# Optimization experiments

Hardware: AMD Instinct MI355X
Metric: run time of the kernel (lower is better)

Reference implementation:

```python
import jax, jax.numpy as jnp
import numpy as np

N_NODES = 100_000
N_EDGES = 2_500_000
HID = 32
SE3_NORM = 1.0 / np.sqrt(32.0)  # e3nn path normalization for 32x0e -> 32x0e


def setup_inputs() -> dict:
    key = jax.random.key(0)
    ks = jax.random.split(key, 14)
    inp = {
        "pos": jax.random.normal(ks[0], (N_NODES, 3), dtype=jnp.float32),
        "edge_index": jax.random.randint(ks[1], (2, N_EDGES), 0, N_NODES, dtype=jnp.int64),
        "Wl1": jax.random.normal(ks[2], (2, HID), dtype=jnp.float32) * 0.5,
        "bl1": jax.random.normal(ks[3], (HID,), dtype=jnp.float32) * 0.1,
        "Wr1": jax.random.normal(ks[4], (2, HID), dtype=jnp.float32) * 0.5,
        "Wl2": jax.random.normal(ks[5], (HID, HID), dtype=jnp.float32) * 0.15,
        "bl2": jax.random.normal(ks[6], (HID,), dtype=jnp.float32) * 0.1,
        "Wr2": jax.random.normal(ks[7], (HID, HID), dtype=jnp.float32) * 0.15,
        "Wse1": jax.random.normal(ks[8], (HID, HID), dtype=jnp.float32) * 0.15,
        "Wse2": jax.random.normal(ks[9], (HID, HID), dtype=jnp.float32) * 0.15,
        "W3": jax.random.normal(ks[10], (HID, HID), dtype=jnp.float32) * 0.15,
        "b3": jax.random.normal(ks[11], (HID,), dtype=jnp.float32) * 0.1,
        "W4": jax.random.normal(ks[12], (HID, 1), dtype=jnp.float32) * 0.15,
        "b4": jax.random.normal(ks[13], (1,), dtype=jnp.float32) * 0.1,
        "alpha": jnp.float32(0.5),
    }
    return inp


def _sage_conv(x, src, dst, Wl, bl, Wr, n_nodes):
    # gather messages from source nodes, scatter-sum onto destination nodes
    agg = jax.ops.segment_sum(x[src], dst, num_segments=n_nodes)  # [N, d_in]
    return agg @ Wl + bl + x @ Wr  # lin_l(agg) + lin_r(x); lin_r has no bias


def reference(pos, edge_index, Wl1, bl1, Wr1, Wl2, bl2, Wr2, Wse1, Wse2, W3, b3, W4, b4, alpha):
    n = pos.shape[0]
    x = pos[:, :2]                       # [N, 2]
    src, dst = edge_index[0], edge_index[1]

    h1 = _sage_conv(x, src, dst, Wl1, bl1, Wr1, n)   # [N, 32]
    h1 = jax.nn.leaky_relu(h1, negative_slope=0.01)  # dropout = identity (eval)
    h1 = (h1 @ Wse1) * SE3_NORM                      # SE3Linear 32x0e->32x0e

    h2 = _sage_conv(h1, src, dst, Wl2, bl2, Wr2, n)
    h2 = jax.nn.leaky_relu(h2, negative_slope=0.01)
    h2 = (h2 @ Wse2) * SE3_NORM

    x_skip = alpha * h1 + h2
    x_out = jax.nn.relu(x_skip @ W3 + b3)            # mlp3 (dropout identity)
    pred = x_out @ W4 + b4                           # mlp4
    return pred.squeeze(-1)                          # [N]
```

## Files before the change

kernel.cpp:

```cpp
#include <hip/hip_runtime.h>
#include <hip/hip_fp16.h>

#define HID 32
#define LEAKY 0.01f
#define SE3NORM 0.17677669529663687f
#define SCAN_TILE 1024
#define NBK 128
#define GA 256
#define NPB2 64


__global__ void k_bhist(const int* __restrict__ ei, int* __restrict__ bh,
                        int E, int B1, int chunk) {
    extern __shared__ int lh[];
    int g = blockIdx.x;
    for (int i = threadIdx.x; i < B1; i += 256) lh[i] = 0;
    __syncthreads();
    int beg = g * chunk, end = min(E, beg + chunk);
    for (int e = beg + (int)threadIdx.x; e < end; e += 256)
        atomicAdd(&lh[ei[E + e] >> 7], 1);
    __syncthreads();
    for (int b = threadIdx.x; b < B1; b += 256) bh[b * GA + g] = lh[b];
}

__global__ void k_scan1(int* __restrict__ data, int* __restrict__ bsum, int M) {
    __shared__ int lds[256];
    int t = threadIdx.x;
    int base = blockIdx.x * SCAN_TILE + t * 4;
    int v0 = (base + 0 < M) ? data[base + 0] : 0;
    int v1 = (base + 1 < M) ? data[base + 1] : 0;
    int v2 = (base + 2 < M) ? data[base + 2] : 0;
    int v3 = (base + 3 < M) ? data[base + 3] : 0;
    int s = v0 + v1 + v2 + v3;
    lds[t] = s;
    __syncthreads();
    for (int off = 1; off < 256; off <<= 1) {
        int x = (t >= off) ? lds[t - off] : 0;
        __syncthreads();
        lds[t] += x;
        __syncthreads();
    }
    int ex = lds[t] - s;
    if (base + 0 < M) data[base + 0] = ex;
    if (base + 1 < M) data[base + 1] = ex + v0;
    if (base + 2 < M) data[base + 2] = ex + v0 + v1;
    if (base + 3 < M) data[base + 3] = ex + v0 + v1 + v2;
    if (t == 255) bsum[blockIdx.x] = lds[255];
}

__global__ void k_scan2(int* __restrict__ bsum, int B) {
    __shared__ int lds[256];
    int t = threadIdx.x;
    int v = (t < B) ? bsum[t] : 0;
    lds[t] = v;
    __syncthreads();
    for (int off = 1; off < 256; off <<= 1) {
        int x = (t >= off) ? lds[t - off] : 0;
        __syncthreads();
        lds[t] += x;
        __syncthreads();
    }
    if (t < B) bsum[t] = lds[t] - v;
}

__global__ void k_scan3(int* __restrict__ data, const int* __restrict__ bsum,
                        int* __restrict__ cursor, int M, int N) {
    int i = blockIdx.x * blockDim.x + threadIdx.x;
    if (i >= M) return;
    int off = data[i] + bsum[i / SCAN_TILE];
    data[i] = off;
    if (cursor && i < N) cursor[i] = off;
}

__global__ void k_bscatter(const int* __restrict__ ei, const int* __restrict__ bh,
                           int* __restrict__ bucketed, int E, int B1, int chunk) {
    extern __shared__ int cur[];
    int g = blockIdx.x;
    for (int b = threadIdx.x; b < B1; b += 256) cur[b] = bh[b * GA + g];
    __syncthreads();
    int beg = g * chunk, end = min(E, beg + chunk);
    for (int e = beg + (int)threadIdx.x; e < end; e += 256) {
        int d = ei[E + e];
        int s = ei[e];
        int b = d >> 7;
        int p = atomicAdd(&cur[b], 1);
        bucketed[p] = s | ((d & (NBK - 1)) << 24);
    }
}

__global__ void k_bsort(const int* __restrict__ bh, const int* __restrict__ bucketed,
                        int* __restrict__ sorted_src, int* __restrict__ offsets,
                        int E, int N, int B1) {
    __shared__ int hist[NBK], sc[NBK], base[NBK];
    int b = blockIdx.x;
    int t = threadIdx.x;
    int bs = bh[b * GA];
    int be = (b == B1 - 1) ? E : bh[(b + 1) * GA];
    if (t < NBK) hist[t] = 0;
    __syncthreads();
    for (int e = bs + t; e < be; e += 256)
        atomicAdd(&hist[bucketed[e] >> 24], 1);
    __syncthreads();
    int v = (t < NBK) ? hist[t] : 0;
    if (t < NBK) sc[t] = v;
    __syncthreads();
    for (int off = 1; off < NBK; off <<= 1) {
        int x = (t < NBK && t >= off) ? sc[t - off] : 0;
        __syncthreads();
        if (t < NBK) sc[t] += x;
        __syncthreads();
    }
    if (t < NBK) base[t] = sc[t] - v;
    __syncthreads();
    if (t < NBK) hist[t] = base[t];
    __syncthreads();
    for (int e = bs + t; e < be; e += 256) {
        int pv = bucketed[e];
        int p = atomicAdd(&hist[pv >> 24], 1);
        sorted_src[bs + p] = pv & 0x00FFFFFF;
    }
    int node = b * NBK + t;
    if (t < NBK && node < N) offsets[node] = bs + base[t];
    if (b == B1 - 1 && t == 0) offsets[N] = E;
}

__global__ void k_hist_rank(const int* __restrict__ ei, int* __restrict__ hist,
                            int* __restrict__ rank, int E) {
    int base = (blockIdx.x * blockDim.x + threadIdx.x) * 4;
#pragma unroll
    for (int u = 0; u < 4; u++) {
        int e = base + u;
        if (e < E) rank[e] = atomicAdd(&hist[ei[E + e]], 1);
    }
}
__global__ void k_hist(const int* __restrict__ ei, int* __restrict__ hist, int E) {
    int base = (blockIdx.x * blockDim.x + threadIdx.x) * 4;
#pragma unroll
    for (int u = 0; u < 4; u++) {
        int e = base + u;
        if (e < E) atomicAdd(&hist[ei[E + e]], 1);
    }
}
__global__ void k_scatter_rank(const int* __restrict__ ei, const int* __restrict__ offsets,
                               const int* __restrict__ rank, int* __restrict__ sorted_src, int E) {
    int base = (blockIdx.x * blockDim.x + threadIdx.x) * 4;
#pragma unroll
    for (int u = 0; u < 4; u++) {
        int e = base + u;
        if (e < E) sorted_src[offsets[ei[E + e]] + rank[e]] = ei[e];
    }
}
__global__ void k_scatter_atomic(const int* __restrict__ ei, int* __restrict__ cursor,
                                 int* __restrict__ sorted_src, int E) {
    int base = (blockIdx.x * blockDim.x + threadIdx.x) * 4;
#pragma unroll
    for (int u = 0; u < 4; u++) {
        int e = base + u;
        if (e < E) {
            int p = atomicAdd(&cursor[ei[E + e]], 1);
            sorted_src[p] = ei[e];
        }
    }
}

__global__ __launch_bounds__(256, 1) void k_node1(
                        const int* __restrict__ offsets, const int* __restrict__ sorted_src,
                        const float* __restrict__ pos,
                        const float* __restrict__ Wl1, const float* __restrict__ bl1,
                        const float* __restrict__ Wr1, const float* __restrict__ Wse1,
                        __half* __restrict__ h1, int N) {
    __shared__ float sWl1[2 * HID], sWr1[2 * HID], sbl1[HID], sWse1[HID * HID];
    __shared__ float sH[32][HID + 4];
    for (int i = threadIdx.x; i < 2 * HID; i += blockDim.x) { sWl1[i] = Wl1[i]; sWr1[i] = Wr1[i]; }
    for (int i = threadIdx.x; i < HID; i += blockDim.x) sbl1[i] = bl1[i];
    for (int i = threadIdx.x; i < HID * HID; i += blockDim.x) sWse1[i] = Wse1[i];
    __syncthreads();

    const int lt = threadIdx.x;
    const int nodeL = lt >> 3;
    const int t = lt & 7;
    const int node = blockIdx.x * 32 + nodeL;
    const bool live = node < N;

    float a0 = 0.f, a1 = 0.f;
    if (live) {
        int beg = offsets[node], end = offsets[node + 1];
        for (int e = beg + t; e < end; e += 8) {
            int s = sorted_src[e];
            a0 += pos[s * 3];
            a1 += pos[s * 3 + 1];
        }
    }
    a0 += __shfl_xor(a0, 1); a1 += __shfl_xor(a1, 1);
    a0 += __shfl_xor(a0, 2); a1 += __shfl_xor(a1, 2);
    a0 += __shfl_xor(a0, 4); a1 += __shfl_xor(a1, 4);

    if (live) {
        float x0 = pos[3 * node], x1 = pos[3 * node + 1];
#pragma unroll
        for (int jj = 0; jj < 4; jj++) {
            int k = t * 4 + jj;
            float v = a0 * sWl1[k] + a1 * sWl1[HID + k] + sbl1[k] + x0 * sWr1[k] + x1 * sWr1[HID + k];
            sH[nodeL][k] = v > 0.f ? v : LEAKY * v;
        }
    }
    __syncthreads();

    if (live) {
        float4 acc = make_float4(0.f, 0.f, 0.f, 0.f);
#pragma unroll 8
        for (int k = 0; k < HID; k++) {
            float hk = sH[nodeL][k];
            float4 w = *(const float4*)&sWse1[k * HID + t * 4];
            acc.x += hk * w.x; acc.y += hk * w.y;
            acc.z += hk * w.z; acc.w += hk * w.w;
        }
        union Pack4 { __half h[4]; float2 v; } p;
        p.h[0] = __float2half(acc.x * SE3NORM);
        p.h[1] = __float2half(acc.y * SE3NORM);
        p.h[2] = __float2half(acc.z * SE3NORM);
        p.h[3] = __float2half(acc.w * SE3NORM);
        *(float2*)&h1[(size_t)node * HID + t * 4] = p.v;
    }
}

__device__ __forceinline__ void acc_h1frag(float2 r, float4& acc) {
    __half2 p01 = __builtin_bit_cast(__half2, r.x);
    __half2 p23 = __builtin_bit_cast(__half2, r.y);
    acc.x += __low2float(p01); acc.y += __high2float(p01);
    acc.z += __low2float(p23); acc.w += __high2float(p23);
}

__global__ __launch_bounds__(512, 1) void k_node2out(
                           const int* __restrict__ offsets, const int* __restrict__ sorted_src,
                           const __half* __restrict__ h1,
                           const float* __restrict__ Wl2, const float* __restrict__ bl2,
                           const float* __restrict__ Wr2, const float* __restrict__ Wse2,
                           const float* __restrict__ W3, const float* __restrict__ b3,
                           const float* __restrict__ W4, const float* __restrict__ b4,
                           const float* __restrict__ alpha_p,
                           float* __restrict__ out, int N) {
    __shared__ float sWl2[HID * HID], sWr2[HID * HID], sWse2[HID * HID], sW3[HID * HID];
    __shared__ float sbl2[HID], sb3[HID], sW4[HID];
    __shared__ float sb4, salpha;
    __shared__ float sA[NPB2][HID + 4], sB[NPB2][HID + 4];
    for (int i = threadIdx.x; i < HID * HID; i += blockDim.x) {
        sWl2[i] = Wl2[i]; sWr2[i] = Wr2[i]; sWse2[i] = Wse2[i]; sW3[i] = W3[i];
    }
    for (int i = threadIdx.x; i < HID; i += blockDim.x) { sbl2[i] = bl2[i]; sb3[i] = b3[i]; sW4[i] = W4[i]; }
    if (threadIdx.x == 0) { sb4 = b4[0]; salpha = alpha_p[0]; }
    __syncthreads();

    const int lt = threadIdx.x;
    const int nodeL = lt >> 3;
    const int t = lt & 7;
    const int node = blockIdx.x * NPB2 + nodeL;
    const bool live = node < N;

    if (live) {
        float2 ro = *(const float2*)&h1[(size_t)node * HID + t * 4];

        int beg = offsets[node], end = offsets[node + 1];
        float4 acc = make_float4(0.f, 0.f, 0.f, 0.f);
        int e = beg;
        for (; e + 8 <= end; e += 8) {
            int s0 = __builtin_nontemporal_load(&sorted_src[e + 0]);
            int s1 = __builtin_nontemporal_load(&sorted_src[e + 1]);
            int s2 = __builtin_nontemporal_load(&sorted_src[e + 2]);
            int s3 = __builtin_nontemporal_load(&sorted_src[e + 3]);
            int s4 = __builtin_nontemporal_load(&sorted_src[e + 4]);
            int s5 = __builtin_nontemporal_load(&sorted_src[e + 5]);
            int s6 = __builtin_nontemporal_load(&sorted_src[e + 6]);
            int s7 = __builtin_nontemporal_load(&sorted_src[e + 7]);
            float2 r0 = *(const float2*)&h1[(size_t)s0 * HID + t * 4];
            float2 r1 = *(const float2*)&h1[(size_t)s1 * HID + t * 4];
            float2 r2 = *(const float2*)&h1[(size_t)s2 * HID + t * 4];
            float2 r3 = *(const float2*)&h1[(size_t)s3 * HID + t * 4];
            float2 r4 = *(const float2*)&h1[(size_t)s4 * HID + t * 4];
            float2 r5 = *(const float2*)&h1[(size_t)s5 * HID + t * 4];
            float2 r6 = *(const float2*)&h1[(size_t)s6 * HID + t * 4];
            float2 r7 = *(const float2*)&h1[(size_t)s7 * HID + t * 4];
            acc_h1frag(r0, acc); acc_h1frag(r1, acc);
            acc_h1frag(r2, acc); acc_h1frag(r3, acc);
            acc_h1frag(r4, acc); acc_h1frag(r5, acc);
            acc_h1frag(r6, acc); acc_h1frag(r7, acc);
        }
        for (; e < end; e++) {
            int s = __builtin_nontemporal_load(&sorted_src[e]);
            float2 r = *(const float2*)&h1[(size_t)s * HID + t * 4];
            acc_h1frag(r, acc);
        }
        __half2 o01 = __builtin_bit_cast(__half2, ro.x);
        __half2 o23 = __builtin_bit_cast(__half2, ro.y);
        float4 own = make_float4(__low2float(o01), __high2float(o01),
                                 __low2float(o23), __high2float(o23));
        *(float4*)&sA[nodeL][t * 4] = acc;
        *(float4*)&sB[nodeL][t * 4] = own;
    }
    __syncthreads();

    float h2r[4];
    if (live) {
        h2r[0] = sbl2[t * 4 + 0]; h2r[1] = sbl2[t * 4 + 1];
        h2r[2] = sbl2[t * 4 + 2]; h2r[3] = sbl2[t * 4 + 3];
#pragma unroll 8
        for (int k = 0; k < HID; k++) {
            float a = sA[nodeL][k];
            float b = sB[nodeL][k];
            float4 wl = *(const float4*)&sWl2[k * HID + t * 4];
            float4 wr = *(const float4*)&sWr2[k * HID + t * 4];
            h2r[0] += a * wl.x + b * wr.x;
            h2r[1] += a * wl.y + b * wr.y;
            h2r[2] += a * wl.z + b * wr.z;
            h2r[3] += a * wl.w + b * wr.w;
        }
#pragma unroll
        for (int jj = 0; jj < 4; jj++) h2r[jj] = h2r[jj] > 0.f ? h2r[jj] : LEAKY * h2r[jj];
    }
    __syncthreads();
    if (live) {
        float4 st = make_float4(h2r[0], h2r[1], h2r[2], h2r[3]);
        *(float4*)&sA[nodeL][t * 4] = st;
    }
    __syncthreads();

    if (live) {
        float4 acc = make_float4(0.f, 0.f, 0.f, 0.f);
#pragma unroll 8
        for (int k = 0; k < HID; k++) {
            float a = sA[nodeL][k];
            float4 w = *(const float4*)&sWse2[k * HID + t * 4];
            acc.x += a * w.x; acc.y += a * w.y;
            acc.z += a * w.z; acc.w += a * w.w;
        }
        float4 own = *(const float4*)&sB[nodeL][t * 4];
        own.x = salpha * own.x + acc.x * SE3NORM;
        own.y = salpha * own.y + acc.y * SE3NORM;
        own.z = salpha * own.z + acc.z * SE3NORM;
        own.w = salpha * own.w + acc.w * SE3NORM;
        *(float4*)&sB[nodeL][t * 4] = own;
    }
    __syncthreads();

    float acc4[4];
    acc4[0] = sb3[t * 4 + 0]; acc4[1] = sb3[t * 4 + 1];
    acc4[2] = sb3[t * 4 + 2]; acc4[3] = sb3[t * 4 + 3];
    if (live) {
#pragma unroll 8
        for (int k = 0; k < HID; k++) {
            float s = sB[nodeL][k];
            float4 w = *(const float4*)&sW3[k * HID + t * 4];
            acc4[0] += s * w.x; acc4[1] += s * w.y;
            acc4[2] += s * w.z; acc4[3] += s * w.w;
        }
    }
    float part = 0.f;
#pragma unroll
    for (int jj = 0; jj < 4; jj++)
        part += (acc4[jj] > 0.f ? acc4[jj] : 0.f) * sW4[t * 4 + jj];
    part += __shfl_xor(part, 1);
    part += __shfl_xor(part, 2);
    part += __shfl_xor(part, 4);
    if (live && t == 0) out[node] = part + sb4;
}

extern "C" void kernel_launch(void* const* d_in, const int* in_sizes, int n_in,
                              void* d_out, int out_size, void* d_ws, size_t ws_size,
                              hipStream_t stream) {
    const float* pos  = (const float*)d_in[0];
    const int*   ei   = (const int*)d_in[1];
    const float* Wl1  = (const float*)d_in[2];
    const float* bl1  = (const float*)d_in[3];
    const float* Wr1  = (const float*)d_in[4];
    const float* Wl2  = (const float*)d_in[5];
    const float* bl2  = (const float*)d_in[6];
    const float* Wr2  = (const float*)d_in[7];
    const float* Wse1 = (const float*)d_in[8];
    const float* Wse2 = (const float*)d_in[9];
    const float* W3   = (const float*)d_in[10];
    const float* b3   = (const float*)d_in[11];
    const float* W4   = (const float*)d_in[12];
    const float* b4   = (const float*)d_in[13];
    const float* alp  = (const float*)d_in[14];
    float* out = (float*)d_out;

    const int N = in_sizes[0] / 3;
    const int E = in_sizes[1] / 2;
    const int blk = 256;
    const size_t h1bytes = (size_t)N * HID * sizeof(__half);

    const int B1 = (N + NBK - 1) / NBK;
    const int M2 = B1 * GA;
    const int S2 = (M2 + SCAN_TILE - 1) / SCAN_TILE;
    {
        int* bh         = (int*)d_ws;
        int* bsum       = bh + M2;
        int* bucketed   = bsum + 256;
        int* sorted_src = bucketed + E;
        int* offsets    = sorted_src + E;
        uintptr_t hp = ((uintptr_t)(offsets + N + 1) + 15) & ~(uintptr_t)15;
        size_t need = (hp - (uintptr_t)d_ws) + h1bytes;
        if (need <= ws_size && S2 <= 256) {
            __half* h1 = (__half*)hp;
            const int chunk = (E + GA - 1) / GA;
            const size_t ldsB = (size_t)B1 * sizeof(int);
            k_bhist<<<GA, 256, ldsB, stream>>>(ei, bh, E, B1, chunk);
            k_scan1<<<S2, 256, 0, stream>>>(bh, bsum, M2);
            k_scan2<<<1, 256, 0, stream>>>(bsum, S2);
            k_scan3<<<(M2 + blk - 1) / blk, blk, 0, stream>>>(bh, bsum, nullptr, M2, 0);
            k_bscatter<<<GA, 256, ldsB, stream>>>(ei, bh, bucketed, E, B1, chunk);
            k_bsort<<<B1, 256, 0, stream>>>(bh, bucketed, sorted_src, offsets, E, N, B1);
            k_node1<<<(N + 31) / 32, 256, 0, stream>>>(offsets, sorted_src, pos,
                                                       Wl1, bl1, Wr1, Wse1, h1, N);
            k_node2out<<<(N + NPB2 - 1) / NPB2, 512, 0, stream>>>(offsets, sorted_src, h1,
                                                          Wl2, bl2, Wr2, Wse2,
                                                          W3, b3, W4, b4, alp, out, N);
            return;
        }
    }

    const int M = N + 1;
    const int B = (M + SCAN_TILE - 1) / SCAN_TILE;
    int* hist       = (int*)d_ws;
    int* offsets    = hist + M;
    int* bsum       = offsets + M;
    int* sorted_src = bsum + 256;
    int* aux        = sorted_src + E;
    uintptr_t hpA = ((uintptr_t)(aux + E) + 15) & ~(uintptr_t)15;
    uintptr_t hpB = ((uintptr_t)(aux + N) + 15) & ~(uintptr_t)15;
    size_t needA = (hpA - (uintptr_t)d_ws) + h1bytes;
    const bool useRank = (needA <= ws_size);
    __half* h1 = (__half*)(useRank ? hpA : hpB);

    hipMemsetAsync(hist, 0, (size_t)M * sizeof(int), stream);
    const int egrid4 = (E / 4 + blk) / blk;
    if (useRank) {
        k_hist_rank<<<egrid4, blk, 0, stream>>>(ei, hist, aux, E);
    } else {
        k_hist<<<egrid4, blk, 0, stream>>>(ei, hist, E);
    }
    k_scan1<<<B, 256, 0, stream>>>(hist, bsum, M);
    k_scan2<<<1, 256, 0, stream>>>(bsum, B);
    k_scan3<<<(M + blk - 1) / blk, blk, 0, stream>>>(hist, bsum, useRank ? nullptr : aux, M, N);
    int* offs = hist;
    if (useRank) {
        k_scatter_rank<<<egrid4, blk, 0, stream>>>(ei, offs, aux, sorted_src, E);
    } else {
        k_scatter_atomic<<<egrid4, blk, 0, stream>>>(ei, aux, sorted_src, E);
    }
    k_node1<<<(N + 31) / 32, 256, 0, stream>>>(offs, sorted_src, pos, Wl1, bl1, Wr1, Wse1, h1, N);
    k_node2out<<<(N + NPB2 - 1) / NPB2, 512, 0, stream>>>(offs, sorted_src, h1, Wl2, bl2, Wr2, Wse2,
                                                  W3, b3, W4, b4, alp, out, N);
}
```

Before: 244.3 us.

## Stage bucket scatter and sort through LDS so global writes land coalesced

Adds a scatter kernel that loads each chunk's destinations into shared memory, locally sorts them by bucket with a counting scan, and then writes the bucketed entries in contiguous runs instead of scattering them at random. The bucket sort kernel likewise stages values in LDS and writes sorted_src sequentially through a permutation. GA grows to 320 so each chunk fits within CHCAP. The cost is extra LDS passes and barriers, plus large LDS use with launch bounds set for one block per SM, which lowers occupancy.

Result: no change. 242.3 us (-0.8%).

```diff
diff --git a/kernel.cpp b/kernel.cpp
--- a/kernel.cpp
+++ b/kernel.cpp
@@ -6,7 +6,8 @@
 #define SE3NORM 0.17677669529663687f
 #define SCAN_TILE 1024
 #define NBK 128
-#define GA 256
+#define GA 320
+#define CHCAP 8192
 #define NPB2 64
 
 
@@ -72,6 +73,69 @@
     if (cursor && i < N) cursor[i] = off;
 }
 
+__global__ __launch_bounds__(256, 1) void k_bscatter2(
+        const int* __restrict__ ei, const int* __restrict__ bh,
+        int* __restrict__ bucketed, int E, int B1, int chunk) {
+    extern __shared__ int lh[];
+    int* cur  = lh;
+    int* hist = lh + B1;
+    int* base = lh + 2 * B1;
+    int* vals = lh + 3 * B1;
+    unsigned short* perm = (unsigned short*)(vals + CHCAP);
+    __shared__ int scanbuf[256];
+    const int g = blockIdx.x;
+    const int t = threadIdx.x;
+    const int beg = g * chunk;
+    const int end = min(E, beg + chunk);
+    const int sz = end - beg;
+
+    for (int b = t; b < B1; b += 256) { cur[b] = bh[b * GA + g]; hist[b] = 0; }
+    __syncthreads();
+    for (int i = t; i < sz; i += 256) {
+        int d = ei[E + beg + i];
+        vals[i] = d;
+        atomicAdd(&hist[d >> 7], 1);
+    }
+    __syncthreads();
+    {
+        int k0 = t * 4;
+        int c0 = (k0 + 0 < B1) ? hist[k0 + 0] : 0;
+        int c1 = (k0 + 1 < B1) ? hist[k0 + 1] : 0;
+        int c2 = (k0 + 2 < B1) ? hist[k0 + 2] : 0;
+        int c3 = (k0 + 3 < B1) ? hist[k0 + 3] : 0;
+        int ssum = c0 + c1 + c2 + c3;
+        scanbuf[t] = ssum;
+        __syncthreads();
+        for (int off = 1; off < 256; off <<= 1) {
+            int x = (t >= off) ? scanbuf[t - off] : 0;
+            __syncthreads();
+            scanbuf[t] += x;
+            __syncthreads();
+        }
+        int ex = scanbuf[t] - ssum;
+        if (k0 + 0 < B1) { base[k0 + 0] = ex; ex += c0; }
+        if (k0 + 1 < B1) { base[k0 + 1] = ex; ex += c1; }
+        if (k0 + 2 < B1) { base[k0 + 2] = ex; ex += c2; }
+        if (k0 + 3 < B1) { base[k0 + 3] = ex; ex += c3; }
+    }
+    __syncthreads();
+    for (int b = t; b < B1; b += 256) hist[b] = base[b];
+    __syncthreads();
+    for (int i = t; i < sz; i += 256) {
+        int bid = vals[i] >> 7;
+        int p = atomicAdd(&hist[bid], 1);
+        perm[p] = (unsigned short)i;
+    }
+    __syncthreads();
+    for (int p = t; p < sz; p += 256) {
+        int i = perm[p];
+        int d = vals[i];
+        int bid = d >> 7;
+        int s = ei[beg + i];
+        bucketed[cur[bid] + (p - base[bid])] = s | ((d & (NBK - 1)) << 24);
+    }
+}
+
 __global__ void k_bscatter(const int* __restrict__ ei, const int* __restrict__ bh,
                            int* __restrict__ bucketed, int E, int B1, int chunk) {
     extern __shared__ int cur[];
@@ -88,36 +152,70 @@
     }
 }
 
-__global__ void k_bsort(const int* __restrict__ bh, const int* __restrict__ bucketed,
-                        int* __restrict__ sorted_src, int* __restrict__ offsets,
-                        int E, int N, int B1) {
+__global__ __launch_bounds__(256, 1) void k_bsort(
+        const int* __restrict__ bh, const int* __restrict__ bucketed,
+        int* __restrict__ sorted_src, int* __restrict__ offsets,
+        int E, int N, int B1) {
     __shared__ int hist[NBK], sc[NBK], base[NBK];
+    __shared__ int vals[CHCAP];
+    __shared__ unsigned short perm[CHCAP];
     int b = blockIdx.x;
     int t = threadIdx.x;
     int bs = bh[b * GA];
     int be = (b == B1 - 1) ? E : bh[(b + 1) * GA];
+    int sz = be - bs;
     if (t < NBK) hist[t] = 0;
     __syncthreads();
-    for (int e = bs + t; e < be; e += 256)
-        atomicAdd(&hist[bucketed[e] >> 24], 1);
-    __syncthreads();
-    int v = (t < NBK) ? hist[t] : 0;
-    if (t < NBK) sc[t] = v;
-    __syncthreads();
-    for (int off = 1; off < NBK; off <<= 1) {
-        int x = (t < NBK && t >= off) ? sc[t - off] : 0;
-        __syncthreads();
-        if (t < NBK) sc[t] += x;
-        __syncthreads();
-    }
-    if (t < NBK) base[t] = sc[t] - v;
-    __syncthreads();
-    if (t < NBK) hist[t] = base[t];
-    __syncthreads();
-    for (int e = bs + t; e < be; e += 256) {
-        int pv = bucketed[e];
-        int p = atomicAdd(&hist[pv >> 24], 1);
-        sorted_src[bs + p] = pv & 0x00FFFFFF;
+
+    if (sz <= CHCAP) {
+        for (int i = t; i < sz; i += 256) {
+            int pv = bucketed[bs + i];
+            vals[i] = pv;
+            atomicAdd(&hist[pv >> 24], 1);
+        }
+        __syncthreads();
+        int v = (t < NBK) ? hist[t] : 0;
+        if (t < NBK) sc[t] = v;
+        __syncthreads();
+        for (int off = 1; off < NBK; off <<= 1) {
+            int x = (t < NBK && t >= off) ? sc[t - off] : 0;
+            __syncthreads();
+            if (t < NBK) sc[t] += x;
+            __syncthreads();
+        }
+        if (t < NBK) base[t] = sc[t] - v;
+        __syncthreads();
+        if (t < NBK) hist[t] = base[t];
+        __syncthreads();
+        for (int i = t; i < sz; i += 256) {
+            int p = atomicAdd(&hist[vals[i] >> 24], 1);
+            perm[p] = (unsigned short)i;
+        }
+        __syncthreads();
+        for (int p = t; p < sz; p += 256)
+            sorted_src[bs + p] = vals[perm[p]] & 0x00FFFFFF;
+    } else {
+        for (int e = bs + t; e < be; e += 256)
+            atomicAdd(&hist[bucketed[e] >> 24], 1);
+        __syncthreads();
+        int v = (t < NBK) ? hist[t] : 0;
+        if (t < NBK) sc[t] = v;
+        __syncthreads();
+        for (int off = 1; off < NBK; off <<= 1) {
+            int x = (t < NBK && t >= off) ? sc[t - off] : 0;
+            __syncthreads();
+            if (t < NBK) sc[t] += x;
+            __syncthreads();
+        }
+        if (t < NBK) base[t] = sc[t] - v;
+        __syncthreads();
+        if (t < NBK) hist[t] = base[t];
+        __syncthreads();
+        for (int e = bs + t; e < be; e += 256) {
+            int pv = bucketed[e];
+            int p = atomicAdd(&hist[pv >> 24], 1);
+            sorted_src[bs + p] = pv & 0x00FFFFFF;
+        }
     }
     int node = b * NBK + t;
     if (t < NBK && node < N) offsets[node] = bs + base[t];
@@ -400,7 +498,7 @@
         int* offsets    = sorted_src + E;
         uintptr_t hp = ((uintptr_t)(offsets + N + 1) + 15) & ~(uintptr_t)15;
         size_t need = (hp - (uintptr_t)d_ws) + h1bytes;
-        if (need <= ws_size && S2 <= 256) {
+        if (need <= ws_size && S2 <= 256 && B1 <= 1024) {
             __half* h1 = (__half*)hp;
             const int chunk = (E + GA - 1) / GA;
             const size_t ldsB = (size_t)B1 * sizeof(int);
@@ -408,7 +506,12 @@
             k_scan1<<<S2, 256, 0, stream>>>(bh, bsum, M2);
             k_scan2<<<1, 256, 0, stream>>>(bsum, S2);
             k_scan3<<<(M2 + blk - 1) / blk, blk, 0, stream>>>(bh, bsum, nullptr, M2, 0);
-            k_bscatter<<<GA, 256, ldsB, stream>>>(ei, bh, bucketed, E, B1, chunk);
+            if (chunk <= CHCAP) {
+                const size_t ldsB2 = (size_t)(3 * B1 + CHCAP) * sizeof(int) + (size_t)CHCAP * sizeof(unsigned short);
+                k_bscatter2<<<GA, 256, ldsB2, stream>>>(ei, bh, bucketed, E, B1, chunk);
+            } else {
+                k_bscatter<<<GA, 256, ldsB, stream>>>(ei, bh, bucketed, E, B1, chunk);
+            }
             k_bsort<<<B1, 256, 0, stream>>>(bh, bucketed, sorted_src, offsets, E, N, B1);
             k_node1<<<(N + 31) / 32, 256, 0, stream>>>(offsets, sorted_src, pos,
                                                        Wl1, bl1, Wr1, Wse1, h1, N);
```
